# Performance work log

Hardware: AMD Instinct MI355X
Metric: run time of the kernel (lower is better)

The kernel has to match this reference:

```python
import jax, jax.numpy as jnp
import numpy as np

N = 50000
E = 800000
F_IN = 128
F_HID = 256   # 2 * out_channels
F_OUT = 128


def setup_inputs() -> dict:
    key = jax.random.key(0)
    ks = jax.random.split(key, 6)
    x = jax.random.normal(ks[0], (N, F_IN), dtype=jnp.float32)
    edge_index = jax.random.randint(ks[1], (2, E), 0, N, dtype=jnp.int64)
    # GCNConv params: glorot weight + zero bias (PyG default)
    s1 = (6.0 / (F_IN + F_HID)) ** 0.5
    s2 = (6.0 / (F_HID + F_OUT)) ** 0.5
    W1 = jax.random.uniform(ks[2], (F_IN, F_HID), jnp.float32, -s1, s1)
    b1 = jnp.zeros((F_HID,), jnp.float32)
    W2 = jax.random.uniform(ks[3], (F_HID, F_OUT), jnp.float32, -s2, s2)
    b2 = jnp.zeros((F_OUT,), jnp.float32)
    return {"x": x, "edge_index": edge_index, "W1": W1, "b1": b1, "W2": W2, "b2": b2}


def _gcn_conv(x, W, b, src, dst, deg_inv_sqrt, n):
    # norm per edge (self-loops already appended to src/dst)
    norm = deg_inv_sqrt[src] * deg_inv_sqrt[dst]          # [E+N]
    h = x @ W                                             # [N, F_out]
    msg = h[src] * norm[:, None]                          # [E+N, F_out] gather
    out = jax.ops.segment_sum(msg, dst, num_segments=n)   # scatter-add
    return out + b


def reference(x, edge_index, W1, b1, W2, b2):
    n = x.shape[0]
    loops = jnp.arange(n, dtype=edge_index.dtype)
    src = jnp.concatenate([edge_index[0], loops])
    dst = jnp.concatenate([edge_index[1], loops])
    # symmetric normalization with self-loops (PyG GCNConv default)
    deg = jax.ops.segment_sum(jnp.ones_like(dst, dtype=x.dtype), dst, num_segments=n)
    deg_inv_sqrt = jnp.where(deg > 0, jax.lax.rsqrt(jnp.maximum(deg, 1e-12)), 0.0)
    h = jax.nn.relu(_gcn_conv(x, W1, b1, src, dst, deg_inv_sqrt, n))
    h = jax.nn.relu(_gcn_conv(h, W2, b2, src, dst, deg_inv_sqrt, n))
    return h
```

## Files before the change

kernel.cpp:

```cpp
#include <hip/hip_runtime.h>


typedef short bf16x8 __attribute__((ext_vector_type(8)));
typedef float f32x4 __attribute__((ext_vector_type(4)));

#define LDSTRIDE 264
#define XTSTRIDE 136
#define BSHIFT 7
#define BMASK 127

__device__ inline unsigned short f2bf(float f) {
    unsigned int u = __float_as_uint(f);
    u += 0x7FFF + ((u >> 16) & 1);
    return (unsigned short)(u >> 16);
}
__device__ inline float bf2f(unsigned short h) {
    return __uint_as_float(((unsigned int)h) << 16);
}

__device__ inline void swz1(const float* W, unsigned short* Ws, int K, int N, int i) {
    int k = i / N, n = i % N;
    int KC = K >> 5;
    size_t d = ((((size_t)(n >> 4) * KC + (k >> 5)) * 64) + ((k >> 3) & 3) * 16 + (n & 15)) * 8
               + (k & 7);
    Ws[d] = f2bf(W[i]);
}
__global__ void wswz_kernel(const float* __restrict__ W1, const float* __restrict__ W2,
                            unsigned short* __restrict__ W1s, unsigned short* __restrict__ W2s,
                            int* __restrict__ ctrl) {
    int i = blockIdx.x * blockDim.x + threadIdx.x;
    if (blockIdx.x == 0) {
        for (int j = threadIdx.x; j < 512; j += 256) ctrl[j] = 0;
    }
    if (i < 32768) swz1(W1, W1s, 128, 256, i);
    else if (i < 65536) swz1(W2, W2s, 256, 128, i - 32768);
}

__global__ __launch_bounds__(256) void bin_kernel(
    const int* __restrict__ src, const int* __restrict__ dst,
    int* __restrict__ bcur, unsigned int* __restrict__ bbuf,
    int E, int cap, int nbuck) {
    __shared__ int cnt[512];
    __shared__ int base[512];
    int t = threadIdx.x;
    for (int i = t; i < nbuck; i += 256) cnt[i] = 0;
    __syncthreads();
    int e0 = blockIdx.x * 2048;
    unsigned int p_[8];
    int b_[8];
#pragma unroll
    for (int i = 0; i < 8; i++) {
        int e = e0 + i * 256 + t;
        if (e < E) {
            int s = src[e], d = dst[e];
            b_[i] = d >> BSHIFT;
            p_[i] = ((unsigned)(d & BMASK) << 24) | (unsigned)s;
            atomicAdd(&cnt[b_[i]], 1);
        } else b_[i] = -1;
    }
    __syncthreads();
    for (int b = t; b < nbuck; b += 256) {
        int c = cnt[b];
        base[b] = (c > 0) ? atomicAdd(&bcur[b], c) : 0;
    }
    __syncthreads();
    for (int i = t; i < nbuck; i += 256) cnt[i] = 0;
    __syncthreads();
#pragma unroll
    for (int i = 0; i < 8; i++) {
        if (b_[i] >= 0) {
            int b = b_[i];
            int p = base[b] + atomicAdd(&cnt[b], 1);
            if (p >= 0 && p < cap) bbuf[(size_t)b * cap + p] = p_[i];
        }
    }
}

__global__ __launch_bounds__(256) void bucket_csr_kernel(
    const int* __restrict__ bcur, const unsigned int* __restrict__ bbuf,
    const float* __restrict__ x,
    int* __restrict__ col, int* __restrict__ rowbeg, int* __restrict__ rowend,
    float* __restrict__ dinv, unsigned short* __restrict__ Xs, int N, int cap) {
    __shared__ int ldeg[128];
    __shared__ int lrp[256];
    __shared__ float sdv[128];
    int b = blockIdx.x, t = threadIdx.x;
    int cnt = min(max(bcur[b], 0), cap);
    if (t < 128) ldeg[t] = 0;
    __syncthreads();
    const unsigned int* mybuf = bbuf + (size_t)b * cap;
    for (int i = t; i < cnt; i += 256)
        atomicAdd(&ldeg[mybuf[i] >> 24], 1);
    __syncthreads();
    int v = (t < 128) ? ldeg[t] : 0;
    lrp[t] = v;
    __syncthreads();
    for (int off = 1; off < 128; off <<= 1) {
        int u = (t >= off) ? lrp[t - off] : 0;
        __syncthreads();
        lrp[t] += u;
        __syncthreads();
    }
    int excl = lrp[t] - v;
    int gbase = b * cap;
    if (t < 128) {
        int r = b * 128 + t;
        float dv = rsqrtf((float)v + 1.0f);
        sdv[t] = dv;
        if (r < N) {
            rowbeg[r] = gbase + excl;
            rowend[r] = gbase + excl + v;
            dinv[r] = dv;
        }
        ldeg[t] = excl;
    }
    __syncthreads();
    for (int i = t; i < cnt; i += 256) {
        unsigned int pr = mybuf[i];
        int p = atomicAdd(&ldeg[pr >> 24], 1);
        col[gbase + p] = (int)(pr & 0xffffffu);
    }
    int rbase = b * 128;
    for (int i = t; i < 128 * 32; i += 256) {
        int rl = i >> 5;
        int gr = rbase + rl;
        if (gr >= N) break;
        float s = sdv[rl];
        float4 xv = ((const float4*)x)[(size_t)gr * 32 + (i & 31)];
        ushort4 o;
        o.x = f2bf(xv.x * s); o.y = f2bf(xv.y * s);
        o.z = f2bf(xv.z * s); o.w = f2bf(xv.w * s);
        ((ushort4*)Xs)[(size_t)gr * 32 + (i & 31)] = o;
    }
}

__global__ __launch_bounds__(256) void gather2_kernel(
    const int* __restrict__ rowbeg, const int* __restrict__ rowend,
    const int* __restrict__ col, const unsigned short* __restrict__ P,
    const float* __restrict__ dinv, const float* __restrict__ bias,
    float* __restrict__ OF, int N) {
    int gid = blockIdx.x * blockDim.x + threadIdx.x;
    int r = gid >> 5;
    if (r >= N) return;
    int lane = gid & 31;
    const size_t off = (size_t)lane * 4;
    const unsigned short* Pf = P + off;

    ushort4 u = *(const ushort4*)(Pf + (size_t)r * 128);
    float ax = bf2f(u.x), ay = bf2f(u.y), az = bf2f(u.z), aw = bf2f(u.w);

    int beg = rowbeg[r], end = rowend[r];
    int i = beg;
    for (; i + 7 < end; i += 8) {
        ushort4 v0 = *(const ushort4*)(Pf + (size_t)col[i + 0] * 128);
        ushort4 v1 = *(const ushort4*)(Pf + (size_t)col[i + 1] * 128);
        ushort4 v2 = *(const ushort4*)(Pf + (size_t)col[i + 2] * 128);
        ushort4 v3 = *(const ushort4*)(Pf + (size_t)col[i + 3] * 128);
        ushort4 v4 = *(const ushort4*)(Pf + (size_t)col[i + 4] * 128);
        ushort4 v5 = *(const ushort4*)(Pf + (size_t)col[i + 5] * 128);
        ushort4 v6 = *(const ushort4*)(Pf + (size_t)col[i + 6] * 128);
        ushort4 v7 = *(const ushort4*)(Pf + (size_t)col[i + 7] * 128);
        ax += bf2f(v0.x) + bf2f(v1.x) + bf2f(v2.x) + bf2f(v3.x)
            + bf2f(v4.x) + bf2f(v5.x) + bf2f(v6.x) + bf2f(v7.x);
        ay += bf2f(v0.y) + bf2f(v1.y) + bf2f(v2.y) + bf2f(v3.y)
            + bf2f(v4.y) + bf2f(v5.y) + bf2f(v6.y) + bf2f(v7.y);
        az += bf2f(v0.z) + bf2f(v1.z) + bf2f(v2.z) + bf2f(v3.z)
            + bf2f(v4.z) + bf2f(v5.z) + bf2f(v6.z) + bf2f(v7.z);
        aw += bf2f(v0.w) + bf2f(v1.w) + bf2f(v2.w) + bf2f(v3.w)
            + bf2f(v4.w) + bf2f(v5.w) + bf2f(v6.w) + bf2f(v7.w);
    }
    for (; i < end; i++) {
        ushort4 a = *(const ushort4*)(Pf + (size_t)col[i] * 128);
        ax += bf2f(a.x); ay += bf2f(a.y); az += bf2f(a.z); aw += bf2f(a.w);
    }
    float s = dinv[r];
    float4 bb = *(const float4*)(bias + off);
    float4 o;
    o.x = fmaxf(ax * s + bb.x, 0.f);
    o.y = fmaxf(ay * s + bb.y, 0.f);
    o.z = fmaxf(az * s + bb.z, 0.f);
    o.w = fmaxf(aw * s + bb.w, 0.f);
    *(float4*)(OF + (size_t)r * 128 + off) = o;
}

__global__ __launch_bounds__(256, 4) void gemm_fused_kernel(
    const int* __restrict__ rowbeg, const int* __restrict__ rowend,
    const int* __restrict__ col, const unsigned short* __restrict__ Xs,
    const unsigned short* __restrict__ W1s, const unsigned short* __restrict__ W2s,
    const float* __restrict__ bias, const float* __restrict__ dinv,
    unsigned short* __restrict__ T, int M) {
    __shared__ unsigned short Xt[16 * XTSTRIDE];
    __shared__ unsigned short Ht[16 * LDSTRIDE];

    int t = threadIdx.x;
    int m0 = blockIdx.x * 16;
    int hw = t >> 5;
    int l  = t & 31;
    const unsigned short* Pf = Xs + (size_t)l * 4;

#pragma unroll
    for (int sub = 0; sub < 2; sub++) {
        int lr = hw * 2 + sub;
        int r = m0 + lr;
        int rc = (r < M) ? r : (M - 1);
        ushort4 u = *(const ushort4*)(Pf + (size_t)rc * 128);
        float ax = bf2f(u.x), ay = bf2f(u.y), az = bf2f(u.z), aw = bf2f(u.w);
        int beg = rowbeg[rc], end = rowend[rc];
        int i = beg;
        for (; i + 7 < end; i += 8) {
            ushort4 v0 = *(const ushort4*)(Pf + (size_t)col[i + 0] * 128);
            ushort4 v1 = *(const ushort4*)(Pf + (size_t)col[i + 1] * 128);
            ushort4 v2 = *(const ushort4*)(Pf + (size_t)col[i + 2] * 128);
            ushort4 v3 = *(const ushort4*)(Pf + (size_t)col[i + 3] * 128);
            ushort4 v4 = *(const ushort4*)(Pf + (size_t)col[i + 4] * 128);
            ushort4 v5 = *(const ushort4*)(Pf + (size_t)col[i + 5] * 128);
            ushort4 v6 = *(const ushort4*)(Pf + (size_t)col[i + 6] * 128);
            ushort4 v7 = *(const ushort4*)(Pf + (size_t)col[i + 7] * 128);
            ax += bf2f(v0.x) + bf2f(v1.x) + bf2f(v2.x) + bf2f(v3.x)
                + bf2f(v4.x) + bf2f(v5.x) + bf2f(v6.x) + bf2f(v7.x);
            ay += bf2f(v0.y) + bf2f(v1.y) + bf2f(v2.y) + bf2f(v3.y)
                + bf2f(v4.y) + bf2f(v5.y) + bf2f(v6.y) + bf2f(v7.y);
            az += bf2f(v0.z) + bf2f(v1.z) + bf2f(v2.z) + bf2f(v3.z)
                + bf2f(v4.z) + bf2f(v5.z) + bf2f(v6.z) + bf2f(v7.z);
            aw += bf2f(v0.w) + bf2f(v1.w) + bf2f(v2.w) + bf2f(v3.w)
                + bf2f(v4.w) + bf2f(v5.w) + bf2f(v6.w) + bf2f(v7.w);
        }
        for (; i < end; i++) {
            ushort4 a = *(const ushort4*)(Pf + (size_t)col[i] * 128);
            ax += bf2f(a.x); ay += bf2f(a.y); az += bf2f(a.z); aw += bf2f(a.w);
        }
        float dvr = dinv[rc];
        ushort4 o;
        o.x = f2bf(ax * dvr); o.y = f2bf(ay * dvr);
        o.z = f2bf(az * dvr); o.w = f2bf(aw * dvr);
        *(ushort4*)(Xt + lr * XTSTRIDE + l * 4) = o;
    }
    __syncthreads();

    int wave = t >> 6;
    int lane = t & 63;
    int mrow = lane & 15, quad = lane >> 4;

    bf16x8 a[4];
#pragma unroll
    for (int kc = 0; kc < 4; kc++)
        a[kc] = *(const bf16x8*)(Xt + mrow * XTSTRIDE + kc * 32 + quad * 8);

    float dv[4];
#pragma unroll
    for (int i2 = 0; i2 < 4; i2++) {
        int gr = m0 + quad * 4 + i2;
        dv[i2] = dinv[gr < M ? gr : M - 1];
    }

    const bf16x8* w1v = (const bf16x8*)W1s;
    for (int nt = wave * 4; nt < wave * 4 + 4; nt++) {
        f32x4 c = {0.f, 0.f, 0.f, 0.f};
#pragma unroll
        for (int kc = 0; kc < 4; kc++) {
            bf16x8 b = w1v[(nt * 4 + kc) * 64 + lane];
            c = __builtin_amdgcn_mfma_f32_16x16x32_bf16(a[kc], b, c, 0, 0, 0);
        }
        int colc = nt * 16 + mrow;
        float bb = bias[colc];
#pragma unroll
        for (int i2 = 0; i2 < 4; i2++) {
            float v = fmaxf(c[i2] + bb, 0.f) * dv[i2];
            Ht[(quad * 4 + i2) * LDSTRIDE + colc] = f2bf(v);
        }
    }
    __syncthreads();

    bf16x8 hh[8];
    const unsigned short* hrow = Ht + mrow * LDSTRIDE + quad * 8;
#pragma unroll
    for (int kc = 0; kc < 8; kc++) hh[kc] = *(const bf16x8*)(hrow + kc * 32);
    const bf16x8* w2v = (const bf16x8*)W2s;
    for (int nt = wave * 2; nt < wave * 2 + 2; nt++) {
        f32x4 c = {0.f, 0.f, 0.f, 0.f};
#pragma unroll
        for (int kc = 0; kc < 8; kc++) {
            bf16x8 b = w2v[(nt * 8 + kc) * 64 + lane];
            c = __builtin_amdgcn_mfma_f32_16x16x32_bf16(hh[kc], b, c, 0, 0, 0);
        }
        int colc = nt * 16 + mrow;
#pragma unroll
        for (int i2 = 0; i2 < 4; i2++) {
            int gr = m0 + quad * 4 + i2;
            if (gr < M) T[(size_t)gr * 128 + colc] = f2bf(c[i2]);
        }
    }
}

extern "C" void kernel_launch(void* const* d_in, const int* in_sizes, int n_in,
                              void* d_out, int out_size, void* d_ws, size_t ws_size,
                              hipStream_t stream) {
    const float* x  = (const float*)d_in[0];
    const int* ei   = (const int*)d_in[1];
    const float* W1 = (const float*)d_in[2];
    const float* b1 = (const float*)d_in[3];
    const float* W2 = (const float*)d_in[4];
    const float* b2 = (const float*)d_in[5];
    float* out      = (float*)d_out;

    const int N = in_sizes[0] / 128;
    const int E = in_sizes[1] / 2;
    const int* src = ei;
    const int* dst = ei + E;

    const int nbuck = (N + BMASK) >> BSHIFT;
    const int cap = E / nbuck + E / (4 * nbuck) + 512;

    float* ws = (float*)d_ws;
    size_t Np = ((size_t)N + 255) & ~(size_t)255;
    float*          dinv = ws;
    unsigned short* Ts   = (unsigned short*)(dinv + Np);
    unsigned short* Xs   = Ts + (size_t)N * 128;
    unsigned short* W1s  = Xs + (size_t)N * 128;
    unsigned short* W2s  = W1s + 32768;
    int* rowbeg = (int*)(W2s + 32768);
    int* rowend = rowbeg + Np;
    int* ctrl   = rowend + Np;
    int* bcur   = ctrl;
    unsigned int* bbuf = (unsigned int*)(ctrl + 512);
    int* col    = (int*)(bbuf + (size_t)nbuck * cap);

    wswz_kernel<<<256, 256, 0, stream>>>(W1, W2, W1s, W2s, ctrl);
    int nbins = (E + 2047) / 2048;
    bin_kernel<<<nbins, 256, 0, stream>>>(src, dst, bcur, bbuf, E, cap, nbuck);
    bucket_csr_kernel<<<nbuck, 256, 0, stream>>>(bcur, bbuf, x, col, rowbeg, rowend,
                                                 dinv, Xs, N, cap);

    int mtiles = (N + 15) / 16;
    gemm_fused_kernel<<<mtiles, 256, 0, stream>>>(rowbeg, rowend, col, Xs,
                                                  W1s, W2s, b1, dinv, Ts, N);

    int gth = N * 32;
    gather2_kernel<<<(gth + 255) / 256, 256, 0, stream>>>(rowbeg, rowend, col, Ts,
                                                          dinv, b2, out, N);
}
```

Baseline: 199.4 us.

## Sort CSR columns, unroll gathers by 16, predicate tails, widen fused GEMM block

Each row's column list is insertion-sorted in the CSR build to make neighbor gathers more cache-friendly. Both gather loops gain a 16-wide unrolled stage with tree-shaped sums, and the scalar tail becomes a predicated 8-wide batch so more loads are in flight at once. The fused GEMM kernel moves to 512 threads with one row per half-wave and fewer MFMA tiles per wave, which raises parallelism during the gather phase. The cost is extra sorting work in the build kernel, higher register pressure, and redundant clamped loads in the tail.

```diff
diff --git a/kernel.cpp b/kernel.cpp
--- a/kernel.cpp
+++ b/kernel.cpp
@@ -120,6 +120,16 @@
         int p = atomicAdd(&ldeg[pr >> 24], 1);
         col[gbase + p] = (int)(pr & 0xffffffu);
     }
+    __syncthreads();
+    if (t < 128) {
+        int s0 = gbase + excl, s1 = gbase + excl + v;
+        for (int a = s0 + 1; a < s1; a++) {
+            int key = col[a];
+            int j = a - 1;
+            while (j >= s0 && col[j] > key) { col[j + 1] = col[j]; j--; }
+            col[j + 1] = key;
+        }
+    }
     int rbase = b * 128;
     for (int i = t; i < 128 * 32; i += 256) {
         int rl = i >> 5;
@@ -134,7 +144,70 @@
     }
 }
 
-__global__ __launch_bounds__(256) void gather2_kernel(
+#define GLOAD16(Pf, col, i)                                                      \
+    ushort4 v0  = *(const ushort4*)((Pf) + (size_t)(col)[(i) + 0]  * 128);       \
+    ushort4 v1  = *(const ushort4*)((Pf) + (size_t)(col)[(i) + 1]  * 128);       \
+    ushort4 v2  = *(const ushort4*)((Pf) + (size_t)(col)[(i) + 2]  * 128);       \
+    ushort4 v3  = *(const ushort4*)((Pf) + (size_t)(col)[(i) + 3]  * 128);       \
+    ushort4 v4  = *(const ushort4*)((Pf) + (size_t)(col)[(i) + 4]  * 128);       \
+    ushort4 v5  = *(const ushort4*)((Pf) + (size_t)(col)[(i) + 5]  * 128);       \
+    ushort4 v6  = *(const ushort4*)((Pf) + (size_t)(col)[(i) + 6]  * 128);       \
+    ushort4 v7  = *(const ushort4*)((Pf) + (size_t)(col)[(i) + 7]  * 128);       \
+    ushort4 v8  = *(const ushort4*)((Pf) + (size_t)(col)[(i) + 8]  * 128);       \
+    ushort4 v9  = *(const ushort4*)((Pf) + (size_t)(col)[(i) + 9]  * 128);       \
+    ushort4 v10 = *(const ushort4*)((Pf) + (size_t)(col)[(i) + 10] * 128);       \
+    ushort4 v11 = *(const ushort4*)((Pf) + (size_t)(col)[(i) + 11] * 128);       \
+    ushort4 v12 = *(const ushort4*)((Pf) + (size_t)(col)[(i) + 12] * 128);       \
+    ushort4 v13 = *(const ushort4*)((Pf) + (size_t)(col)[(i) + 13] * 128);       \
+    ushort4 v14 = *(const ushort4*)((Pf) + (size_t)(col)[(i) + 14] * 128);       \
+    ushort4 v15 = *(const ushort4*)((Pf) + (size_t)(col)[(i) + 15] * 128);       \
+    ax += ((bf2f(v0.x) + bf2f(v1.x)) + (bf2f(v2.x) + bf2f(v3.x)))               \
+        + ((bf2f(v4.x) + bf2f(v5.x)) + (bf2f(v6.x) + bf2f(v7.x)))               \
+        + ((bf2f(v8.x) + bf2f(v9.x)) + (bf2f(v10.x) + bf2f(v11.x)))             \
+        + ((bf2f(v12.x) + bf2f(v13.x)) + (bf2f(v14.x) + bf2f(v15.x)));          \
+    ay += ((bf2f(v0.y) + bf2f(v1.y)) + (bf2f(v2.y) + bf2f(v3.y)))               \
+        + ((bf2f(v4.y) + bf2f(v5.y)) + (bf2f(v6.y) + bf2f(v7.y)))               \
+        + ((bf2f(v8.y) + bf2f(v9.y)) + (bf2f(v10.y) + bf2f(v11.y)))             \
+        + ((bf2f(v12.y) + bf2f(v13.y)) + (bf2f(v14.y) + bf2f(v15.y)));          \
+    az += ((bf2f(v0.z) + bf2f(v1.z)) + (bf2f(v2.z) + bf2f(v3.z)))               \
+        + ((bf2f(v4.z) + bf2f(v5.z)) + (bf2f(v6.z) + bf2f(v7.z)))               \
+        + ((bf2f(v8.z) + bf2f(v9.z)) + (bf2f(v10.z) + bf2f(v11.z)))             \
+        + ((bf2f(v12.z) + bf2f(v13.z)) + (bf2f(v14.z) + bf2f(v15.z)));          \
+    aw += ((bf2f(v0.w) + bf2f(v1.w)) + (bf2f(v2.w) + bf2f(v3.w)))               \
+        + ((bf2f(v4.w) + bf2f(v5.w)) + (bf2f(v6.w) + bf2f(v7.w)))               \
+        + ((bf2f(v8.w) + bf2f(v9.w)) + (bf2f(v10.w) + bf2f(v11.w)))             \
+        + ((bf2f(v12.w) + bf2f(v13.w)) + (bf2f(v14.w) + bf2f(v15.w)));
+
+#define GTAIL8(Pf, col, i, end)                                                  \
+    if ((i) < (end)) {                                                           \
+        int cl = (end) - 1;                                                      \
+        int e1 = (i) + 1 < (end) ? (i) + 1 : cl, e2 = (i) + 2 < (end) ? (i) + 2 : cl; \
+        int e3 = (i) + 3 < (end) ? (i) + 3 : cl, e4 = (i) + 4 < (end) ? (i) + 4 : cl; \
+        int e5 = (i) + 5 < (end) ? (i) + 5 : cl, e6 = (i) + 6 < (end) ? (i) + 6 : cl; \
+        int e7 = (i) + 7 < (end) ? (i) + 7 : cl;                                 \
+        float m1 = (i) + 1 < (end) ? 1.f : 0.f, m2 = (i) + 2 < (end) ? 1.f : 0.f; \
+        float m3 = (i) + 3 < (end) ? 1.f : 0.f, m4 = (i) + 4 < (end) ? 1.f : 0.f; \
+        float m5 = (i) + 5 < (end) ? 1.f : 0.f, m6 = (i) + 6 < (end) ? 1.f : 0.f; \
+        float m7 = (i) + 7 < (end) ? 1.f : 0.f;                                  \
+        ushort4 t0 = *(const ushort4*)((Pf) + (size_t)(col)[(i)] * 128);         \
+        ushort4 t1 = *(const ushort4*)((Pf) + (size_t)(col)[e1] * 128);          \
+        ushort4 t2 = *(const ushort4*)((Pf) + (size_t)(col)[e2] * 128);          \
+        ushort4 t3 = *(const ushort4*)((Pf) + (size_t)(col)[e3] * 128);          \
+        ushort4 t4 = *(const ushort4*)((Pf) + (size_t)(col)[e4] * 128);          \
+        ushort4 t5 = *(const ushort4*)((Pf) + (size_t)(col)[e5] * 128);          \
+        ushort4 t6 = *(const ushort4*)((Pf) + (size_t)(col)[e6] * 128);          \
+        ushort4 t7 = *(const ushort4*)((Pf) + (size_t)(col)[e7] * 128);          \
+        ax += bf2f(t0.x) + m1 * bf2f(t1.x) + m2 * bf2f(t2.x) + m3 * bf2f(t3.x)  \
+            + m4 * bf2f(t4.x) + m5 * bf2f(t5.x) + m6 * bf2f(t6.x) + m7 * bf2f(t7.x); \
+        ay += bf2f(t0.y) + m1 * bf2f(t1.y) + m2 * bf2f(t2.y) + m3 * bf2f(t3.y)  \
+            + m4 * bf2f(t4.y) + m5 * bf2f(t5.y) + m6 * bf2f(t6.y) + m7 * bf2f(t7.y); \
+        az += bf2f(t0.z) + m1 * bf2f(t1.z) + m2 * bf2f(t2.z) + m3 * bf2f(t3.z)  \
+            + m4 * bf2f(t4.z) + m5 * bf2f(t5.z) + m6 * bf2f(t6.z) + m7 * bf2f(t7.z); \
+        aw += bf2f(t0.w) + m1 * bf2f(t1.w) + m2 * bf2f(t2.w) + m3 * bf2f(t3.w)  \
+            + m4 * bf2f(t4.w) + m5 * bf2f(t5.w) + m6 * bf2f(t6.w) + m7 * bf2f(t7.w); \
+    }
+
+__global__ __launch_bounds__(256, 3) void gather2_kernel(
     const int* __restrict__ rowbeg, const int* __restrict__ rowend,
     const int* __restrict__ col, const unsigned short* __restrict__ P,
     const float* __restrict__ dinv, const float* __restrict__ bias,
@@ -151,6 +224,7 @@
 
     int beg = rowbeg[r], end = rowend[r];
     int i = beg;
+    for (; i + 15 < end; i += 16) { GLOAD16(Pf, col, i) }
     for (; i + 7 < end; i += 8) {
         ushort4 v0 = *(const ushort4*)(Pf + (size_t)col[i + 0] * 128);
         ushort4 v1 = *(const ushort4*)(Pf + (size_t)col[i + 1] * 128);
@@ -160,19 +234,16 @@
         ushort4 v5 = *(const ushort4*)(Pf + (size_t)col[i + 5] * 128);
         ushort4 v6 = *(const ushort4*)(Pf + (size_t)col[i + 6] * 128);
         ushort4 v7 = *(const ushort4*)(Pf + (size_t)col[i + 7] * 128);
-        ax += bf2f(v0.x) + bf2f(v1.x) + bf2f(v2.x) + bf2f(v3.x)
-            + bf2f(v4.x) + bf2f(v5.x) + bf2f(v6.x) + bf2f(v7.x);
-        ay += bf2f(v0.y) + bf2f(v1.y) + bf2f(v2.y) + bf2f(v3.y)
-            + bf2f(v4.y) + bf2f(v5.y) + bf2f(v6.y) + bf2f(v7.y);
-        az += bf2f(v0.z) + bf2f(v1.z) + bf2f(v2.z) + bf2f(v3.z)
-            + bf2f(v4.z) + bf2f(v5.z) + bf2f(v6.z) + bf2f(v7.z);
-        aw += bf2f(v0.w) + bf2f(v1.w) + bf2f(v2.w) + bf2f(v3.w)
-            + bf2f(v4.w) + bf2f(v5.w) + bf2f(v6.w) + bf2f(v7.w);
-    }
-    for (; i < end; i++) {
-        ushort4 a = *(const ushort4*)(Pf + (size_t)col[i] * 128);
-        ax += bf2f(a.x); ay += bf2f(a.y); az += bf2f(a.z); aw += bf2f(a.w);
-    }
+        ax += (bf2f(v0.x) + bf2f(v1.x)) + (bf2f(v2.x) + bf2f(v3.x))
+            + (bf2f(v4.x) + bf2f(v5.x)) + (bf2f(v6.x) + bf2f(v7.x));
+        ay += (bf2f(v0.y) + bf2f(v1.y)) + (bf2f(v2.y) + bf2f(v3.y))
+            + (bf2f(v4.y) + bf2f(v5.y)) + (bf2f(v6.y) + bf2f(v7.y));
+        az += (bf2f(v0.z) + bf2f(v1.z)) + (bf2f(v2.z) + bf2f(v3.z))
+            + (bf2f(v4.z) + bf2f(v5.z)) + (bf2f(v6.z) + bf2f(v7.z));
+        aw += (bf2f(v0.w) + bf2f(v1.w)) + (bf2f(v2.w) + bf2f(v3.w))
+            + (bf2f(v4.w) + bf2f(v5.w)) + (bf2f(v6.w) + bf2f(v7.w));
+    }
+    GTAIL8(Pf, col, i, end)
     float s = dinv[r];
     float4 bb = *(const float4*)(bias + off);
     float4 o;
@@ -183,7 +254,7 @@
     *(float4*)(OF + (size_t)r * 128 + off) = o;
 }
 
-__global__ __launch_bounds__(256, 4) void gemm_fused_kernel(
+__global__ __launch_bounds__(512, 3) void gemm_fused_kernel(
     const int* __restrict__ rowbeg, const int* __restrict__ rowend,
     const int* __restrict__ col, const unsigned short* __restrict__ Xs,
     const unsigned short* __restrict__ W1s, const unsigned short* __restrict__ W2s,
@@ -198,15 +269,14 @@
     int l  = t & 31;
     const unsigned short* Pf = Xs + (size_t)l * 4;
 
-#pragma unroll
-    for (int sub = 0; sub < 2; sub++) {
-        int lr = hw * 2 + sub;
-        int r = m0 + lr;
+    {
+        int r = m0 + hw;
         int rc = (r < M) ? r : (M - 1);
         ushort4 u = *(const ushort4*)(Pf + (size_t)rc * 128);
         float ax = bf2f(u.x), ay = bf2f(u.y), az = bf2f(u.z), aw = bf2f(u.w);
         int beg = rowbeg[rc], end = rowend[rc];
         int i = beg;
+        for (; i + 15 < end; i += 16) { GLOAD16(Pf, col, i) }
         for (; i + 7 < end; i += 8) {
             ushort4 v0 = *(const ushort4*)(Pf + (size_t)col[i + 0] * 128);
             ushort4 v1 = *(const ushort4*)(Pf + (size_t)col[i + 1] * 128);
@@ -216,24 +286,21 @@
             ushort4 v5 = *(const ushort4*)(Pf + (size_t)col[i + 5] * 128);
             ushort4 v6 = *(const ushort4*)(Pf + (size_t)col[i + 6] * 128);
             ushort4 v7 = *(const ushort4*)(Pf + (size_t)col[i + 7] * 128);
-            ax += bf2f(v0.x) + bf2f(v1.x) + bf2f(v2.x) + bf2f(v3.x)
-                + bf2f(v4.x) + bf2f(v5.x) + bf2f(v6.x) + bf2f(v7.x);
-            ay += bf2f(v0.y) + bf2f(v1.y) + bf2f(v2.y) + bf2f(v3.y)
-                + bf2f(v4.y) + bf2f(v5.y) + bf2f(v6.y) + bf2f(v7.y);
-            az += bf2f(v0.z) + bf2f(v1.z) + bf2f(v2.z) + bf2f(v3.z)
-                + bf2f(v4.z) + bf2f(v5.z) + bf2f(v6.z) + bf2f(v7.z);
-            aw += bf2f(v0.w) + bf2f(v1.w) + bf2f(v2.w) + bf2f(v3.w)
-                + bf2f(v4.w) + bf2f(v5.w) + bf2f(v6.w) + bf2f(v7.w);
-        }
-        for (; i < end; i++) {
-            ushort4 a = *(const ushort4*)(Pf + (size_t)col[i] * 128);
-            ax += bf2f(a.x); ay += bf2f(a.y); az += bf2f(a.z); aw += bf2f(a.w);
-        }
+            ax += (bf2f(v0.x) + bf2f(v1.x)) + (bf2f(v2.x) + bf2f(v3.x))
+                + (bf2f(v4.x) + bf2f(v5.x)) + (bf2f(v6.x) + bf2f(v7.x));
+            ay += (bf2f(v0.y) + bf2f(v1.y)) + (bf2f(v2.y) + bf2f(v3.y))
+                + (bf2f(v4.y) + bf2f(v5.y)) + (bf2f(v6.y) + bf2f(v7.y));
+            az += (bf2f(v0.z) + bf2f(v1.z)) + (bf2f(v2.z) + bf2f(v3.z))
+                + (bf2f(v4.z) + bf2f(v5.z)) + (bf2f(v6.z) + bf2f(v7.z));
+            aw += (bf2f(v0.w) + bf2f(v1.w)) + (bf2f(v2.w) + bf2f(v3.w))
+                + (bf2f(v4.w) + bf2f(v5.w)) + (bf2f(v6.w) + bf2f(v7.w));
+        }
+        GTAIL8(Pf, col, i, end)
         float dvr = dinv[rc];
         ushort4 o;
         o.x = f2bf(ax * dvr); o.y = f2bf(ay * dvr);
         o.z = f2bf(az * dvr); o.w = f2bf(aw * dvr);
-        *(ushort4*)(Xt + lr * XTSTRIDE + l * 4) = o;
+        *(ushort4*)(Xt + hw * XTSTRIDE + l * 4) = o;
     }
     __syncthreads();
 
@@ -254,7 +321,7 @@
     }
 
     const bf16x8* w1v = (const bf16x8*)W1s;
-    for (int nt = wave * 4; nt < wave * 4 + 4; nt++) {
+    for (int nt = wave * 2; nt < wave * 2 + 2; nt++) {
         f32x4 c = {0.f, 0.f, 0.f, 0.f};
 #pragma unroll
         for (int kc = 0; kc < 4; kc++) {
@@ -276,7 +343,8 @@
 #pragma unroll
     for (int kc = 0; kc < 8; kc++) hh[kc] = *(const bf16x8*)(hrow + kc * 32);
     const bf16x8* w2v = (const bf16x8*)W2s;
-    for (int nt = wave * 2; nt < wave * 2 + 2; nt++) {
+    {
+        int nt = wave;
         f32x4 c = {0.f, 0.f, 0.f, 0.f};
 #pragma unroll
         for (int kc = 0; kc < 8; kc++) {
@@ -332,7 +400,7 @@
                                                  dinv, Xs, N, cap);
 
     int mtiles = (N + 15) / 16;
-    gemm_fused_kernel<<<mtiles, 256, 0, stream>>>(rowbeg, rowend, col, Xs,
+    gemm_fused_kernel<<<mtiles, 512, 0, stream>>>(rowbeg, rowend, col, Xs,
                                                   W1s, W2s, b1, dinv, Ts, N);
 
     int gth = N * 32;
```

Measured after the change: 276.3 us. 1.39x slower.
